# Performance work log

Hardware: AMD Instinct MI355X
Metric: run time of the kernel (lower is better)

## Reference

```python
import jax, jax.numpy as jnp
import numpy as np

FEATURE_DIM = 512
NUM_HEADS = 8
HEAD_DIM = FEATURE_DIM // NUM_HEADS


def setup_inputs() -> dict:
    key = jax.random.key(0)
    ks = jax.random.split(key, 16)
    B, N, F = 16, 768, FEATURE_DIM
    Nb = N // 3
    s = 1.0 / np.sqrt(F)
    inp = {
        "x_1": jax.random.normal(ks[0], (B, N, F), jnp.float32),
        "x_2": jax.random.normal(ks[1], (B, N, F), jnp.float32),
        "z_b": jax.random.normal(ks[2], (Nb, F), jnp.float32),
        # weights stored [in, out] (torch Linear applies x @ W.T)
        "Wqkv_i": jax.random.normal(ks[3], (F, 3 * F), jnp.float32) * s,
        "Wqkv_j": jax.random.normal(ks[4], (F, 3 * F), jnp.float32) * s,
        "Wqkv_b": jax.random.normal(ks[5], (F, 3 * F), jnp.float32) * s,
        "W_f": jax.random.normal(ks[6], (2 * F, F), jnp.float32) * s,
        "b_f": jnp.zeros((F,), jnp.float32),
        "W_m": jax.random.normal(ks[7], (F, F), jnp.float32) * s,
        "b_m": jnp.zeros((F,), jnp.float32),
        "W_QKV": jax.random.normal(ks[8], (F, 3 * F), jnp.float32) * s,
        "W_proj": jax.random.normal(ks[9], (F, F), jnp.float32) * s,
        "b_proj": jnp.zeros((F,), jnp.float32),
    }
    return inp


def reference(x_1, x_2, z_b, Wqkv_i, Wqkv_j, Wqkv_b, W_f, b_f, W_m, b_m, W_QKV, W_proj, b_proj):
    z_i, z_j = x_1, x_2
    B, N, F = z_i.shape
    Nb = z_b.shape[0]
    scale = F ** -0.5           # full-dim attention scale
    Scale = HEAD_DIM ** -0.5    # multi-head attention scale

    zb = jnp.broadcast_to((z_b * 0.2)[None], (B, Nb, F))

    def split_qkv(x, W):
        qkv = (x @ W).reshape(x.shape[0], x.shape[1], 3, F)
        return qkv[:, :, 0], qkv[:, :, 1], qkv[:, :, 2]

    _, k_i, v_i = split_qkv(z_i, Wqkv_i)
    q_j, _, _ = split_qkv(z_j, Wqkv_j)
    q_b, k_b, v_b = split_qkv(zb, Wqkv_b)

    # bottleneck cross attentions (single-head, full feature dim)
    a_ib = jax.nn.softmax(jnp.einsum('bmf,bnf->bmn', q_b, k_i) * scale, axis=-1)  # [B,Nb,N]
    a_bj = jax.nn.softmax(jnp.einsum('bnf,bmf->bnm', q_j, k_b) * scale, axis=-1)  # [B,N,Nb]

    a_ib = jnp.einsum('bmn,bnf->bmf', a_ib, v_i)  # [B,Nb,F]
    attn_up = jax.nn.softmax(jnp.einsum('bnf,bmf->bnm', z_i, a_ib) * scale, axis=-1)  # [B,N,Nb]
    a_ib = jnp.einsum('bnm,bmf->bnf', attn_up, a_ib)  # [B,N,F]
    a_bj = jnp.einsum('bnm,bmf->bnf', a_bj, v_b)      # [B,N,F]
    a_ij = (a_ib + a_bj) * 0.5

    # gated fusion
    f_ij = jax.nn.sigmoid(jnp.concatenate([a_ij, z_j], axis=-1) @ W_f + b_f)
    h_ij = jax.nn.relu(z_i + (a_ij @ W_m + b_m) * f_ij)

    # standard multi-head self-attention
    QKV = (h_ij @ W_QKV).reshape(B, N, 3, NUM_HEADS, HEAD_DIM)
    Q, K, V = [jnp.transpose(QKV[:, :, t], (0, 2, 1, 3)) for t in range(3)]  # [B,H,N,hd]
    Attn = jax.nn.softmax(jnp.einsum('bhnd,bhmd->bhnm', Q, K) * Scale, axis=-1)
    H = jnp.einsum('bhnm,bhmd->bhnd', Attn, V)
    H = jnp.transpose(H, (0, 2, 1, 3)).reshape(B, N, F)
    return H @ W_proj + b_proj
```

## Files before the change

kernel.cpp:

```cpp
#include <hip/hip_runtime.h>
#include <hip/hip_bf16.h>

typedef __attribute__((ext_vector_type(8))) short short8;
typedef __attribute__((ext_vector_type(4))) float f32x4;
typedef __hip_bfloat16 bf16;
typedef unsigned short ushort;

__device__ __forceinline__ ushort f2b(float v) {
    bf16 h = __float2bfloat16(v);
    return *reinterpret_cast<ushort*>(&h);
}
__device__ __forceinline__ float b2f(ushort u) {
    return __uint_as_float((unsigned)u << 16);
}

#define GLD16(lds, gp) __builtin_amdgcn_global_load_lds( \
    (const __attribute__((address_space(1))) void*)(gp), \
    (__attribute__((address_space(3))) void*)(lds), 16, 0, 0)

__device__ __forceinline__ void xcd_swizzle(int& bx, int& by) {
    if ((gridDim.y & 7) == 0) {
        const int id = bx + gridDim.x * by;
        const int xcd = id & 7, slot = id >> 3;
        by = xcd * (gridDim.y >> 3) + slot / gridDim.x;
        bx = slot - (slot / gridDim.x) * gridDim.x;
    }
}

template<typename OutT, int EPI, int TM>
__global__ __launch_bounds__(256) void gemm_bf16(
    const bf16* __restrict__ A, const bf16* __restrict__ B, OutT* __restrict__ C,
    int K, int lda, int ldb, int ldc, long sA, long sB, long sC,
    float alpha, const float* __restrict__ bias,
    int lda2, long sA2, int eld, long sE,
    bf16* __restrict__ px, bf16* __restrict__ py, int nry)
{
    constexpr int RT = TM / 32;
    constexpr int PLA = TM * 32;
    constexpr int PLB = 128 * 32;
    constexpr int NP = (TM == 64) ? 4 : 2;
    __shared__ __align__(16) bf16 As[NP * PLA];
    __shared__ __align__(16) bf16 Bs[NP * PLB];

    const int t = threadIdx.x;
    const int w = t >> 6, lane = t & 63;
    const int wr = w >> 1, wc = w & 1;
    const int lr = lane & 15, kc4 = lane >> 4;
    const int qr = lane >> 2;
    const int kcr = ((lane & 3) - ((lane >> 3) & 3)) & 3;
    int bx = blockIdx.x, by = blockIdx.y;
    xcd_swizzle(bx, by);
    int zidx, row0;
    if (nry > 0) { zidx = by / nry; row0 = (by % nry) * TM; }
    else         { zidx = blockIdx.z; row0 = by * TM; }
    const int col0 = bx * 128;

    const bf16* Asel = A; const bf16* Bsel = B;
    long sBe = sB, sAe = sA; int ldbe = ldb, ldae = lda;
    if constexpr (EPI == 7) {
        if (blockIdx.z == 1) {
            Asel = (const bf16*)px; Bsel = (const bf16*)py;
            sBe = 0; ldbe = eld; ldae = lda2; sAe = sA2;
        }
    }
    const bf16* Ab = Asel + (size_t)zidx * sAe + (size_t)row0 * ldae;
    const bf16* Bb = Bsel + (size_t)zidx * sBe + (size_t)col0 * ldbe;

    const bf16* ga0; const bf16* ga1 = nullptr;
    if constexpr (TM == 64) {
        ga0 = Ab + (size_t)(w * 16 + qr) * ldae + kcr * 8;
    } else {
        ga0 = Ab + (size_t)(w * 32 + qr) * ldae + kcr * 8;
        ga1 = Ab + (size_t)(w * 32 + 16 + qr) * ldae + kcr * 8;
    }
    const bf16* gb0 = Bb + (size_t)(w * 32 + qr) * ldbe + kcr * 8;
    const bf16* gb1 = Bb + (size_t)(w * 32 + 16 + qr) * ldbe + kcr * 8;
    bf16* lA0; bf16* lA1 = nullptr;
    if constexpr (TM == 64) { lA0 = &As[w * 512]; }
    else                    { lA0 = &As[w * 1024]; lA1 = &As[w * 1024 + 512]; }
    bf16* lB0 = &Bs[w * 1024];
    bf16* lB1 = &Bs[w * 1024 + 512];

    f32x4 acc[RT][4] = {};

    const int cSw = ((kc4 + ((lr >> 1) & 3)) & 3) * 8;
    const bf16* ApBase = &As[(wr * (TM / 2) + lr) * 32 + cSw];
    const bf16* BpBase = &Bs[(wc * 64 + lr) * 32 + cSw];

    auto stageP = [&](int plane, int ko) {
        GLD16(lA0 + plane * PLA, ga0 + ko);
        if constexpr (TM == 128) GLD16(lA1 + plane * PLA, ga1 + ko);
        GLD16(lB0 + plane * PLB, gb0 + ko);
        GLD16(lB1 + plane * PLB, gb1 + ko);
    };
    auto compP = [&](int plane) {
        const bf16* Ap = ApBase + plane * PLA;
        const bf16* Bp = BpBase + plane * PLB;
        short8 af[RT], bfr[4];
#pragma unroll
        for (int i = 0; i < RT; ++i) af[i]  = *(const short8*)(Ap + i * 512);
#pragma unroll
        for (int j = 0; j < 4; ++j) bfr[j] = *(const short8*)(Bp + j * 512);
#pragma unroll
        for (int i = 0; i < RT; ++i)
#pragma unroll
            for (int j = 0; j < 4; ++j)
                acc[i][j] = __builtin_amdgcn_mfma_f32_16x16x32_bf16(af[i], bfr[j], acc[i][j], 0, 0, 0);
    };

    if constexpr (TM == 64) {
        stageP(0, 0); stageP(1, 32);
        int buf = 0;
        for (int k0 = 0; k0 < K; k0 += 64) {
            __syncthreads();
            if (k0 + 64 < K) {
                stageP((buf ^ 1) * 2,     k0 + 64);
                stageP((buf ^ 1) * 2 + 1, k0 + 96);
            }
            compP(buf * 2); compP(buf * 2 + 1);
            buf ^= 1;
        }
    } else {
        stageP(0, 0);
        int buf = 0;
        for (int k0 = 0; k0 < K; k0 += 32) {
            __syncthreads();
            if (k0 + 32 < K) stageP(buf ^ 1, k0 + 32);
            compP(buf);
            buf ^= 1;
        }
    }

    if constexpr (EPI == 4) {
        const int sec = bx >> 2;
        const int h0 = (bx & 3) * 2;
        const int b  = by / 6;
        const int n0 = (by % 6) * TM;
        bf16* dq = (bf16*)C;
#pragma unroll
        for (int j = 0; j < 4; ++j) {
            const int col = wc * 64 + j * 16 + lr;
            const int h = h0 + (col >> 6), hd = col & 63;
            const size_t bh = (size_t)b * 8 + h;
#pragma unroll
            for (int i = 0; i < RT; ++i) {
                const int n = n0 + wr * (TM / 2) + i * 16 + kc4 * 4;
                if (sec == 2) {
                    __align__(8) ushort o[4];
#pragma unroll
                    for (int r = 0; r < 4; ++r) o[r] = f2b(acc[i][j][r]);
                    *(int2*)&py[(bh * 64 + hd) * 768 + n] = *(const int2*)o;
                } else {
                    bf16* d = (sec == 0) ? dq : px;
#pragma unroll
                    for (int r = 0; r < 4; ++r)
                        d[(bh * 768 + n + r) * 64 + hd] = __float2bfloat16(acc[i][j][r]);
                }
            }
        }
        return;
    } else if constexpr (EPI == 5) {
        const int b  = by / 6;
        const int n0 = (by % 6) * TM;
#pragma unroll
        for (int j = 0; j < 4; ++j) {
            const int col = col0 + wc * 64 + j * 16 + lr;
#pragma unroll
            for (int i = 0; i < RT; ++i) {
                const int n = n0 + wr * (TM / 2) + i * 16 + kc4 * 4;
                if (col < 512) {
#pragma unroll
                    for (int r = 0; r < 4; ++r)
                        ((bf16*)C)[((size_t)b * 768 + n + r) * 512 + col] = __float2bfloat16(acc[i][j][r]);
                } else {
                    __align__(8) ushort o[4];
#pragma unroll
                    for (int r = 0; r < 4; ++r) o[r] = f2b(acc[i][j][r]);
                    *(int2*)&py[((size_t)b * 512 + (col - 512)) * 768 + n] = *(const int2*)o;
                }
            }
        }
        return;
    }

    const int czid = (EPI == 7) ? (int)blockIdx.z * 16 + zidx : zidx;
    OutT* Cb = C + (size_t)czid * sC;
#pragma unroll
    for (int j = 0; j < 4; ++j) {
        const int col = col0 + wc * 64 + j * 16 + lr;
        const float bv = bias ? bias[col] : 0.f;
#pragma unroll
        for (int i = 0; i < RT; ++i) {
            const int rb = row0 + wr * (TM / 2) + i * 16 + kc4 * 4;
            if constexpr (EPI == 6) {
                __align__(8) ushort o[4];
#pragma unroll
                for (int r = 0; r < 4; ++r) {
                    o[r] = f2b(alpha * acc[i][j][r]);
                    Cb[(size_t)(rb + r) * ldc + col] = __float2bfloat16(alpha * acc[i][j][r]);
                }
                *(int2*)&py[(size_t)czid * sE + (size_t)col * eld + rb] = *(const int2*)o;
            } else if constexpr (EPI == 8) {
                __align__(8) ushort o[4];
#pragma unroll
                for (int r = 0; r < 4; ++r) {
                    o[r] = f2b(acc[i][j][r]);
                    Cb[(size_t)(rb + r) * ldc + col] = __float2bfloat16(acc[i][j][r]);
                }
                if (col >= 1024) {
                    const size_t tb = (size_t)(col - 1024) * 512 + 256 + rb;
#pragma unroll
                    for (int b2 = 0; b2 < 16; ++b2)
                        *(int2*)&py[(size_t)b2 * sE + tb] = *(const int2*)o;
                }
            } else {
#pragma unroll
                for (int r = 0; r < 4; ++r) {
                    const int row = rb + r;
                    float v = alpha * acc[i][j][r] + bv;
                    if constexpr (sizeof(OutT) == 2)
                        Cb[(size_t)row * ldc + col] = __float2bfloat16(v);
                    else
                        Cb[(size_t)row * ldc + col] = v;
                }
            }
        }
    }
}

__global__ __launch_bounds__(256) void gemm_gate(
    const bf16* __restrict__ A, const bf16* __restrict__ Bf,
    const bf16* __restrict__ Bm, bf16* __restrict__ Cout,
    const float* __restrict__ bias_f, const float* __restrict__ bias_m,
    const float* __restrict__ x1)
{
    constexpr int AHW = 64 * 32;
    constexpr int BHW = 128 * 32;
    __shared__ __align__(16) bf16 As[2 * AHW];
    __shared__ __align__(16) bf16 FsS[2 * BHW];
    __shared__ __align__(16) bf16 MsS[2 * BHW];

    const int t = threadIdx.x;
    const int w = t >> 6, lane = t & 63;
    const int lr = lane & 15, kc4 = lane >> 4;
    const int qr = lane >> 2;
    const int kcr = ((lane & 3) - ((lane >> 3) & 3)) & 3;
    int bx = blockIdx.x, by = blockIdx.y;
    xcd_swizzle(bx, by);
    const int row0 = by * 64, col0 = bx * 128;

    const bf16* ga0 = A  + (size_t)(row0 + w * 16 + qr) * 1024 + kcr * 8;
    const bf16* gf0 = Bf + (size_t)(col0 + w * 32 + qr) * 1024 + kcr * 8;
    const bf16* gf1 = Bf + (size_t)(col0 + w * 32 + 16 + qr) * 1024 + kcr * 8;
    const bf16* gm0 = Bm + (size_t)(col0 + w * 32 + qr) * 512 + kcr * 8;
    const bf16* gm1 = Bm + (size_t)(col0 + w * 32 + 16 + qr) * 512 + kcr * 8;
    bf16* lA0 = &As[w * 512];
    bf16* lF0 = &FsS[w * 1024]; bf16* lF1 = &FsS[w * 1024 + 512];
    bf16* lM0 = &MsS[w * 1024]; bf16* lM1 = &MsS[w * 1024 + 512];

    f32x4 acc1[4][2] = {};
    f32x4 acc2[4][2] = {};

    const int cSw = ((kc4 + ((lr >> 1) & 3)) & 3) * 8;
    const bf16* ApBase = &As[lr * 32 + cSw];
    const bf16* FpBase = &FsS[(w * 32 + lr) * 32 + cSw];
    const bf16* MpBase = &MsS[(w * 32 + lr) * 32 + cSw];

    GLD16(lA0, ga0);
    GLD16(lF0, gf0); GLD16(lF1, gf1);
    GLD16(lM0, gm0); GLD16(lM1, gm1);

    auto step = [&](int kk, int rd, int st) {
        __syncthreads();
        const int kn = kk + 32;
        if (kn < 1024) {
            GLD16(lA0 + st * AHW, ga0 + kn);
            GLD16(lF0 + st * BHW, gf0 + kn);
            GLD16(lF1 + st * BHW, gf1 + kn);
            if (kn < 512) {
                GLD16(lM0 + st * BHW, gm0 + kn);
                GLD16(lM1 + st * BHW, gm1 + kn);
            }
        }
        const bf16* Ap = ApBase + rd * AHW;
        const bf16* Fp = FpBase + rd * BHW;
        short8 af[4], ff[2];
#pragma unroll
        for (int i = 0; i < 4; ++i) af[i] = *(const short8*)(Ap + i * 512);
#pragma unroll
        for (int j = 0; j < 2; ++j) ff[j] = *(const short8*)(Fp + j * 512);
#pragma unroll
        for (int i = 0; i < 4; ++i)
#pragma unroll
            for (int j = 0; j < 2; ++j)
                acc1[i][j] = __builtin_amdgcn_mfma_f32_16x16x32_bf16(af[i], ff[j], acc1[i][j], 0, 0, 0);
        if (kk < 512) {
            const bf16* Mp = MpBase + rd * BHW;
            short8 mf[2];
#pragma unroll
            for (int j = 0; j < 2; ++j) mf[j] = *(const short8*)(Mp + j * 512);
#pragma unroll
            for (int i = 0; i < 4; ++i)
#pragma unroll
                for (int j = 0; j < 2; ++j)
                    acc2[i][j] = __builtin_amdgcn_mfma_f32_16x16x32_bf16(af[i], mf[j], acc2[i][j], 0, 0, 0);
        }
    };

    for (int k0 = 0; k0 < 1024; k0 += 64) {
        step(k0, 0, 1);
        step(k0 + 32, 1, 0);
    }

#pragma unroll
    for (int j = 0; j < 2; ++j) {
        const int col = col0 + w * 32 + j * 16 + lr;
        const float bvf = bias_f[col], bvm = bias_m[col];
#pragma unroll
        for (int i = 0; i < 4; ++i) {
            const int rb = row0 + i * 16 + kc4 * 4;
#pragma unroll
            for (int r = 0; r < 4; ++r) {
                const int row = rb + r;
                const float sig = 1.f / (1.f + __expf(-(acc1[i][j][r] + bvf)));
                const float rr = x1[(size_t)row * 512 + col] + (acc2[i][j][r] + bvm) * sig;
                Cout[(size_t)row * 512 + col] = __float2bfloat16(rr > 0.f ? rr : 0.f);
            }
        }
    }
}

template<typename TI, int NSRC>
__global__ __launch_bounds__(256) void k_transpose(
    const TI* __restrict__ s0, const TI* __restrict__ s1,
    const TI* __restrict__ s2, const TI* __restrict__ s3,
    bf16* __restrict__ dst, int src_ld, int dst_ld, long sSrc, long sDst,
    int rep, long repStride)
{
    __shared__ float tile[64][65];
    const int t = threadIdx.x;
    const int c0 = blockIdx.x * 64, r0 = blockIdx.y * 64;
    const int z = blockIdx.z;
    const TI* src = s0;
    if (NSRC > 1) src = (z == 0) ? s0 : (z == 1) ? s1 : (z == 2) ? s2 : s3;
    {
        const int r = t >> 2, cq = (t & 3) * 16;
        const TI* sp = src + (size_t)z * sSrc + (size_t)(r0 + r) * src_ld + c0 + cq;
        if constexpr (sizeof(TI) == 4) {
#pragma unroll
            for (int u = 0; u < 16; u += 4) {
                float4 v = *(const float4*)((const float*)sp + u);
                tile[r][cq + u]     = v.x; tile[r][cq + u + 1] = v.y;
                tile[r][cq + u + 2] = v.z; tile[r][cq + u + 3] = v.w;
            }
        } else {
            const ushort* up = (const ushort*)sp;
            union { short8 v; ushort u[8]; } p0, p1;
            p0.v = *(const short8*)up; p1.v = *(const short8*)(up + 8);
#pragma unroll
            for (int u = 0; u < 8; ++u) {
                tile[r][cq + u]     = b2f(p0.u[u]);
                tile[r][cq + 8 + u] = b2f(p1.u[u]);
            }
        }
    }
    __syncthreads();
    const int c = t >> 2, rq = (t & 3) * 16;
    __align__(16) ushort ob[16];
#pragma unroll
    for (int u = 0; u < 16; ++u) ob[u] = f2b(tile[rq + u][c]);
    for (int rp = 0; rp < rep; ++rp) {
        bf16* dp = dst + (size_t)rp * repStride + (size_t)z * sDst + (size_t)(c0 + c) * dst_ld + r0 + rq;
        *(int4*)dp       = *(const int4*)&ob[0];
        *(int4*)(dp + 8) = *(const int4*)&ob[8];
    }
}

__global__ __launch_bounds__(256) void k_cast3(const float* __restrict__ x1,
    const float* __restrict__ x2, const float* __restrict__ zb,
    const float* __restrict__ wj,
    bf16* __restrict__ d1, bf16* __restrict__ d2, bf16* __restrict__ d3,
    bf16* __restrict__ d4)
{
    const int z = blockIdx.z;
    const float* src; bf16* dst; int ld; float scale; int n;
    if (z == 0)      { src = x1; dst = d1; ld = 512;  scale = 1.f;  n = 6291456; }
    else if (z == 1) { src = x2; dst = d2; ld = 1024; scale = 1.f;  n = 6291456; }
    else if (z == 2) { src = zb; dst = d3; ld = 512;  scale = 0.2f; n = 131072;  }
    else             { src = wj; dst = d4; ld = 512;  scale = 1.f;  n = 262144;  }
    int i = (blockIdx.x * 256 + threadIdx.x) * 8;
    if (i >= n) return;
    int si = i;
    if (z == 3) si = (i >> 9) * 1536 + (i & 511);
    float4 a = *(const float4*)(src + si), b = *(const float4*)(src + si + 4);
    __align__(16) ushort o[8];
    o[0] = f2b(a.x * scale); o[1] = f2b(a.y * scale); o[2] = f2b(a.z * scale); o[3] = f2b(a.w * scale);
    o[4] = f2b(b.x * scale); o[5] = f2b(b.y * scale); o[6] = f2b(b.z * scale); o[7] = f2b(b.w * scale);
    int row = i >> 9, col = i & 511;
    *(int4*)(dst + (size_t)row * ld + col) = *(const int4*)o;
}

template<int COLS, int MODE>
__global__ __launch_bounds__(256) void softmax_wave(const float* __restrict__ X,
                                                    bf16* __restrict__ Y)
{
    const int wv = threadIdx.x >> 6, lane = threadIdx.x & 63;
    const long row = (long)blockIdx.x * 4 + wv;
    const float* src = X + row * COLS;
    constexpr int V = COLS / 64;
    float v[V];
#pragma unroll
    for (int i = 0; i < V; ++i) v[i] = src[lane + i * 64];
    float m = v[0];
#pragma unroll
    for (int i = 1; i < V; ++i) m = fmaxf(m, v[i]);
#pragma unroll
    for (int o = 32; o; o >>= 1) m = fmaxf(m, __shfl_xor(m, o));
    float s = 0.f;
#pragma unroll
    for (int i = 0; i < V; ++i) { v[i] = __expf(v[i] - m); s += v[i]; }
#pragma unroll
    for (int o = 32; o; o >>= 1) s += __shfl_xor(s, o);
    const float inv = 1.f / s;
    bf16* dst;
    if constexpr (MODE == 0) {
        dst = Y + row * COLS;
    } else {
        const int z = (int)(row / 768), mm = (int)(row % 768);
        dst = Y + ((size_t)(z & 15) * 768 + mm) * 512 + (z >> 4) * 256;
    }
#pragma unroll
    for (int i = 0; i < V; ++i) dst[lane + i * 64] = __float2bfloat16(v[i] * inv);
}

__global__ __launch_bounds__(256) void mhsa_flash_mfma(
    const bf16* __restrict__ Qb, const bf16* __restrict__ Kb,
    const bf16* __restrict__ VT, bf16* __restrict__ Hout)
{
    constexpr int LD = 72;
    __shared__ __align__(16) ushort Qs[64 * LD];
    __shared__ __align__(16) ushort Ks[64 * LD];
    __shared__ __align__(16) ushort Vt[64 * LD];
    __shared__ __align__(16) ushort Ps[64 * LD];

    const int t = threadIdx.x;
    const int w = t >> 6, lane = t & 63;
    const int l16 = lane & 15, q4 = lane >> 4;
    const int h = blockIdx.x, b = blockIdx.y, qt = blockIdx.z;
    const size_t bh = (size_t)b * 8 + h;
    const ushort* qbase = (const ushort*)Qb + bh * 768 * 64;
    const ushort* kbase = (const ushort*)Kb + bh * 768 * 64;
    const ushort* vbase = (const ushort*)VT + bh * 64 * 768;

    const int r = t >> 2, c0 = (t & 3) * 16;

    {
        const ushort* src = qbase + (size_t)(qt * 64 + r) * 64 + c0;
        *(int4*)&Qs[r * LD + c0]     = *(const int4*)src;
        *(int4*)&Qs[r * LD + c0 + 8] = *(const int4*)(src + 8);
    }

    int4 ka0, ka1, va0, va1;
    {
        const ushort* ks = kbase + (size_t)r * 64 + c0;
        ka0 = *(const int4*)ks; ka1 = *(const int4*)(ks + 8);
        const ushort* vs = vbase + (size_t)r * 768 + c0;
        va0 = *(const int4*)vs; va1 = *(const int4*)(vs + 8);
    }
    __syncthreads();

    short8 qf0 = *(const short8*)&Qs[(w * 16 + l16) * LD + q4 * 8];
    short8 qf1 = *(const short8*)&Qs[(w * 16 + l16) * LD + 32 + q4 * 8];

    float lsum[4] = {0.f, 0.f, 0.f, 0.f};
    f32x4 acc[4] = {};

    for (int kt = 0; kt < 12; ++kt) {
        if (kt) __syncthreads();
        *(int4*)&Ks[r * LD + c0]     = ka0;
        *(int4*)&Ks[r * LD + c0 + 8] = ka1;
        *(int4*)&Vt[r * LD + c0]     = va0;
        *(int4*)&Vt[r * LD + c0 + 8] = va1;
        __syncthreads();

        if (kt < 11) {
            const ushort* ks = kbase + (size_t)((kt + 1) * 64 + r) * 64 + c0;
            ka0 = *(const int4*)ks; ka1 = *(const int4*)(ks + 8);
            const ushort* vs = vbase + (size_t)r * 768 + (kt + 1) * 64 + c0;
            va0 = *(const int4*)vs; va1 = *(const int4*)(vs + 8);
        }

        f32x4 s[4] = {};
#pragma unroll
        for (int nt = 0; nt < 4; ++nt) {
            short8 kf0 = *(const short8*)&Ks[(nt * 16 + l16) * LD + q4 * 8];
            short8 kf1 = *(const short8*)&Ks[(nt * 16 + l16) * LD + 32 + q4 * 8];
            s[nt] = __builtin_amdgcn_mfma_f32_16x16x32_bf16(qf0, kf0, s[nt], 0, 0, 0);
            s[nt] = __builtin_amdgcn_mfma_f32_16x16x32_bf16(qf1, kf1, s[nt], 0, 0, 0);
        }

#pragma unroll
        for (int nt = 0; nt < 4; ++nt) {
#pragma unroll
            for (int e = 0; e < 4; ++e) {
                const float p = __expf(s[nt][e] * 0.125f);
                lsum[e] += p;
                Ps[(w * 16 + q4 * 4 + e) * LD + nt * 16 + l16] = f2b(p);
            }
        }

        short8 pf0 = *(const short8*)&Ps[(w * 16 + l16) * LD + q4 * 8];
        short8 pf1 = *(const short8*)&Ps[(w * 16 + l16) * LD + 32 + q4 * 8];
#pragma unroll
        for (int jt = 0; jt < 4; ++jt) {
            short8 vf0 = *(const short8*)&Vt[(jt * 16 + l16) * LD + q4 * 8];
            short8 vf1 = *(const short8*)&Vt[(jt * 16 + l16) * LD + 32 + q4 * 8];
            acc[jt] = __builtin_amdgcn_mfma_f32_16x16x32_bf16(pf0, vf0, acc[jt], 0, 0, 0);
            acc[jt] = __builtin_amdgcn_mfma_f32_16x16x32_bf16(pf1, vf1, acc[jt], 0, 0, 0);
        }
    }

    const int orow = qt * 64 + w * 16 + q4 * 4;
#pragma unroll
    for (int e = 0; e < 4; ++e) {
        float l = lsum[e];
        l += __shfl_xor(l, 1);
        l += __shfl_xor(l, 2);
        l += __shfl_xor(l, 4);
        l += __shfl_xor(l, 8);
        const float inv = 1.f / l;
        const size_t rbase = ((size_t)b * 768 + orow + e) * 512 + h * 64;
#pragma unroll
        for (int jt = 0; jt < 4; ++jt)
            Hout[rbase + jt * 16 + l16] = __float2bfloat16(acc[jt][e] * inv);
    }
}

extern "C" void kernel_launch(void* const* d_in, const int* in_sizes, int n_in,
                              void* d_out, int out_size, void* d_ws, size_t ws_size,
                              hipStream_t stream)
{
    (void)in_sizes; (void)n_in; (void)out_size; (void)ws_size;
    const float* x1     = (const float*)d_in[0];
    const float* x2     = (const float*)d_in[1];
    const float* z_b    = (const float*)d_in[2];
    const float* Wqkv_i = (const float*)d_in[3];
    const float* Wqkv_j = (const float*)d_in[4];
    const float* Wqkv_b = (const float*)d_in[5];
    const float* W_f    = (const float*)d_in[6];
    const float* b_f    = (const float*)d_in[7];
    const float* W_m    = (const float*)d_in[8];
    const float* b_m    = (const float*)d_in[9];
    const float* W_QKV  = (const float*)d_in[10];
    const float* W_proj = (const float*)d_in[11];
    const float* b_proj = (const float*)d_in[12];
    float* out = (float*)d_out;

    const float scale = 0.044194173824159216f;

    char* base = (char*)d_ws;
    size_t off = 0;
    auto alloc = [&](size_t bytes) { char* r = base + off; off += (bytes + 255) & ~(size_t)255; return r; };

    char* Rq  = alloc((size_t)3 * 25165824);
    char* R1  = Rq;
    char* R2  = Rq + 25165824;
    char* R3  = Rq + 2 * 25165824;
    char* R4  = alloc(25165824);
    bf16* Wt4     = (bf16*)alloc((size_t)3 * 1536 * 512 * 2);
    bf16* Wt_f    = (bf16*)alloc(512 * 1024 * 2);
    bf16* Wt_mp   = (bf16*)alloc((size_t)2 * 512 * 512 * 2);
    bf16* Wj_bf   = (bf16*)alloc(512 * 512 * 2);
    bf16* Gbuf    = (bf16*)alloc(256 * 512 * 2);
    bf16* c_zb    = (bf16*)alloc(256 * 512 * 2);
    bf16* qkvb    = (bf16*)alloc(256 * 1536 * 2);
    bf16* aib0    = (bf16*)alloc((size_t)16 * 256 * 512 * 2);
    bf16* Bcat    = (bf16*)alloc((size_t)16 * 512 * 512 * 2);
    float* S      = (float*)alloc((size_t)32 * 768 * 256 * 4);
    bf16* Sb1     = (bf16*)alloc((size_t)16 * 256 * 768 * 2);
    bf16* Sb_cat  = (bf16*)alloc((size_t)16 * 768 * 512 * 2);
    bf16* c_cat   = (bf16*)alloc((size_t)12288 * 1024 * 2);
    bf16* hbuf    = (bf16*)alloc((size_t)12288 * 512 * 2);

    bf16* Wt_i = Wt4, *Wt_b = Wt4 + 1536 * 512,
        *Wt_qkv = Wt4 + (size_t)2 * 1536 * 512;
    bf16* Wt_m = Wt_mp, *Wt_proj = Wt_mp + 512 * 512;

    bf16*  Kc   = (bf16*)R1;
    bf16*  Qb   = (bf16*)R1;
    bf16*  Kb   = (bf16*)(R1 + 12582912);
    bf16*  v_iT = (bf16*)R2;
    bf16*  VTb  = (bf16*)R2;
    bf16*  c_x1 = (bf16*)R3;
    bf16*  Hout = (bf16*)R4;

    auto G64 = [&](const bf16* A, const bf16* B, void* C, bool outBf,
                   int M, int N, int K, int lda, int ldb, int ldc,
                   long sA, long sB, long sC, int batch, float alpha,
                   const float* bias) {
        int nry = M / 64;
        dim3 grid(N / 128, (batch > 1) ? batch * nry : nry, 1);
        if (batch == 1) nry = 0;
        if (outBf) gemm_bf16<bf16, 0, 64><<<grid, 256, 0, stream>>>(A, B, (bf16*)C, K, lda, ldb, ldc, sA, sB, sC, alpha, bias, 0, 0, 0, 0, nullptr, nullptr, nry);
        else       gemm_bf16<float, 0, 64><<<grid, 256, 0, stream>>>(A, B, (float*)C, K, lda, ldb, ldc, sA, sB, sC, alpha, bias, 0, 0, 0, 0, nullptr, nullptr, nry);
    };

    k_cast3<<<dim3(3072, 1, 4), 256, 0, stream>>>(x1, x2, z_b, Wqkv_j,
                                                  c_x1, c_cat + 512, c_zb, Wj_bf);
    k_transpose<float, 3><<<dim3(24, 8, 3), 256, 0, stream>>>(
        Wqkv_i, Wqkv_b, W_QKV, nullptr, Wt4, 1536, 512, 0, 1536L * 512, 1, 0);
    k_transpose<float, 1><<<dim3(8, 16, 1), 256, 0, stream>>>(
        W_f, nullptr, nullptr, nullptr, Wt_f, 512, 1024, 0, 0, 1, 0);
    k_transpose<float, 2><<<dim3(8, 8, 2), 256, 0, stream>>>(
        W_m, W_proj, nullptr, nullptr, Wt_mp, 512, 512, 0, 512L * 512, 1, 0);

    gemm_bf16<bf16, 8, 64><<<dim3(12, 4, 1), 256, 0, stream>>>(
        c_zb, Wt_b, qkvb, 512, 512, 512, 1536, 0, 0, 0,
        1.f, nullptr, 0, 0, 0, 512L * 512, nullptr, Bcat, 0);
    G64(qkvb + 512, Wj_bf, Gbuf, true, 256, 512, 512, 1536, 512, 512, 0, 0, 0, 1, 1.f, nullptr);
    gemm_bf16<bf16, 5, 128><<<dim3(8, 96, 1), 256, 0, stream>>>(
        c_x1, Wt_i + 512 * 512, Kc, 512, 512, 512, 512, 0, 0, 0,
        1.f, nullptr, 0, 0, 0, 0, nullptr, v_iT, 0);
    G64(qkvb, Kc, S, false, 256, 768, 512, 1536, 512, 768, 0, 768L * 512, 256L * 768, 16, scale, nullptr);
    softmax_wave<768, 0><<<1024, 256, 0, stream>>>(S, Sb1);
    gemm_bf16<bf16, 6, 64><<<dim3(4, 64, 1), 256, 0, stream>>>(
        Sb1, v_iT, aib0, 768, 768, 768, 512, 256L * 768, 512L * 768, 256L * 512,
        1.f, nullptr, 0, 0, 512, 512L * 512, nullptr, Bcat, 4);
    gemm_bf16<float, 7, 64><<<dim3(2, 192, 2), 256, 0, stream>>>(
        c_x1, aib0, S, 512, 512, 512, 256, 768L * 512, 256L * 512, 768L * 256,
        scale, nullptr, 1024, 768L * 1024, 512, 0,
        c_cat + 512, Gbuf, 12);
    softmax_wave<256, 1><<<6144, 256, 0, stream>>>(S, Sb_cat);
    G64(Sb_cat, Bcat, c_cat, true, 768, 512, 512, 512, 512, 1024,
        768L * 512, 512L * 512, 768L * 1024, 16, 0.5f, nullptr);
    gemm_gate<<<dim3(4, 192), 256, 0, stream>>>(c_cat, Wt_f, Wt_m, hbuf, b_f, b_m, x1);
    gemm_bf16<bf16, 4, 128><<<dim3(12, 96, 1), 256, 0, stream>>>(
        hbuf, Wt_qkv, Qb, 512, 512, 512, 0, 0, 0, 0,
        1.f, nullptr, 0, 0, 0, 0, Kb, VTb, 0);
    mhsa_flash_mfma<<<dim3(8, 16, 12), 256, 0, stream>>>(Qb, Kb, VTb, Hout);
    G64(Hout, Wt_proj, out, false, 12288, 512, 512, 512, 512, 512, 0, 0, 0, 1, 1.f, b_proj);
}
```

Measured before the change: 382.4 us.

## Fuse attn_up/bottleneck score GEMM with row softmax into one kernel

Replaces the EPI-7 GEMM that wrote fp32 scores to a scratch buffer, and the separate 256-wide softmax pass, with a new gemm_sm kernel. Each block computes a full 64x256 score tile across two waves per row and combines max and sum through shared memory. It then writes normalized bf16 probabilities straight into Sb_cat, removing the fp32 round trip and one launch. The gate kernel also reads x1 from the existing bf16 copy instead of fp32, which cuts bandwidth but slightly lowers precision of the residual.

```diff
diff --git a/kernel.cpp b/kernel.cpp
--- a/kernel.cpp
+++ b/kernel.cpp
@@ -55,26 +55,18 @@
     else         { zidx = blockIdx.z; row0 = by * TM; }
     const int col0 = bx * 128;
 
-    const bf16* Asel = A; const bf16* Bsel = B;
-    long sBe = sB, sAe = sA; int ldbe = ldb, ldae = lda;
-    if constexpr (EPI == 7) {
-        if (blockIdx.z == 1) {
-            Asel = (const bf16*)px; Bsel = (const bf16*)py;
-            sBe = 0; ldbe = eld; ldae = lda2; sAe = sA2;
-        }
-    }
-    const bf16* Ab = Asel + (size_t)zidx * sAe + (size_t)row0 * ldae;
-    const bf16* Bb = Bsel + (size_t)zidx * sBe + (size_t)col0 * ldbe;
+    const bf16* Ab = A + (size_t)zidx * sA + (size_t)row0 * lda;
+    const bf16* Bb = B + (size_t)zidx * sB + (size_t)col0 * ldb;
 
     const bf16* ga0; const bf16* ga1 = nullptr;
     if constexpr (TM == 64) {
-        ga0 = Ab + (size_t)(w * 16 + qr) * ldae + kcr * 8;
+        ga0 = Ab + (size_t)(w * 16 + qr) * lda + kcr * 8;
     } else {
-        ga0 = Ab + (size_t)(w * 32 + qr) * ldae + kcr * 8;
-        ga1 = Ab + (size_t)(w * 32 + 16 + qr) * ldae + kcr * 8;
-    }
-    const bf16* gb0 = Bb + (size_t)(w * 32 + qr) * ldbe + kcr * 8;
-    const bf16* gb1 = Bb + (size_t)(w * 32 + 16 + qr) * ldbe + kcr * 8;
+        ga0 = Ab + (size_t)(w * 32 + qr) * lda + kcr * 8;
+        ga1 = Ab + (size_t)(w * 32 + 16 + qr) * lda + kcr * 8;
+    }
+    const bf16* gb0 = Bb + (size_t)(w * 32 + qr) * ldb + kcr * 8;
+    const bf16* gb1 = Bb + (size_t)(w * 32 + 16 + qr) * ldb + kcr * 8;
     bf16* lA0; bf16* lA1 = nullptr;
     if constexpr (TM == 64) { lA0 = &As[w * 512]; }
     else                    { lA0 = &As[w * 1024]; lA1 = &As[w * 1024 + 512]; }
@@ -183,8 +175,7 @@
         return;
     }
 
-    const int czid = (EPI == 7) ? (int)blockIdx.z * 16 + zidx : zidx;
-    OutT* Cb = C + (size_t)czid * sC;
+    OutT* Cb = C + (size_t)zidx * sC;
 #pragma unroll
     for (int j = 0; j < 4; ++j) {
         const int col = col0 + wc * 64 + j * 16 + lr;
@@ -199,7 +190,7 @@
                     o[r] = f2b(alpha * acc[i][j][r]);
                     Cb[(size_t)(rb + r) * ldc + col] = __float2bfloat16(alpha * acc[i][j][r]);
                 }
-                *(int2*)&py[(size_t)czid * sE + (size_t)col * eld + rb] = *(const int2*)o;
+                *(int2*)&py[(size_t)zidx * sE + (size_t)col * eld + rb] = *(const int2*)o;
             } else if constexpr (EPI == 8) {
                 __align__(8) ushort o[4];
 #pragma unroll
@@ -228,11 +219,134 @@
     }
 }
 
+__global__ __launch_bounds__(256) void gemm_sm(
+    const bf16* __restrict__ A0, const bf16* __restrict__ B0,
+    const bf16* __restrict__ A1, const bf16* __restrict__ B1,
+    bf16* __restrict__ Y, float alpha)
+{
+    constexpr int PLA = 64 * 32;
+    constexpr int PLB = 256 * 32;
+    __shared__ __align__(16) bf16 As[2 * PLA];
+    __shared__ __align__(16) bf16 Bs[2 * PLB];
+    __shared__ float sc[2][2][2][32];
+
+    const int t = threadIdx.x;
+    const int w = t >> 6, lane = t & 63;
+    const int wr = w >> 1, wc = w & 1;
+    const int lr = lane & 15, kc4 = lane >> 4;
+    const int qr = lane >> 2;
+    const int kcr = ((lane & 3) - ((lane >> 3) & 3)) & 3;
+    int bx = blockIdx.x, by = blockIdx.y;
+    xcd_swizzle(bx, by);
+    const int b = by / 12, row0 = (by % 12) * 64;
+    const int half = blockIdx.z;
+
+    const bf16* Ab; int lda; const bf16* Bb;
+    if (half == 0) {
+        Ab = A0 + (size_t)b * (768L * 512) + (size_t)row0 * 512;  lda = 512;
+        Bb = B0 + (size_t)b * (256L * 512);
+    } else {
+        Ab = A1 + (size_t)b * (768L * 1024) + (size_t)row0 * 1024; lda = 1024;
+        Bb = B1;
+    }
+
+    const bf16* ga0 = Ab + (size_t)(w * 16 + qr) * lda + kcr * 8;
+    const bf16* gb0 = Bb + (size_t)(w * 32 + qr) * 512 + kcr * 8;
+    const bf16* gb1 = Bb + (size_t)(w * 32 + 16 + qr) * 512 + kcr * 8;
+    const bf16* gb2 = Bb + (size_t)(128 + w * 32 + qr) * 512 + kcr * 8;
+    const bf16* gb3 = Bb + (size_t)(128 + w * 32 + 16 + qr) * 512 + kcr * 8;
+    bf16* lA0 = &As[w * 512];
+    bf16* lB0 = &Bs[w * 1024];        bf16* lB1 = &Bs[w * 1024 + 512];
+    bf16* lB2 = &Bs[4096 + w * 1024]; bf16* lB3 = &Bs[4096 + w * 1024 + 512];
+
+    f32x4 acc[2][8] = {};
+
+    const int cSw = ((kc4 + ((lr >> 1) & 3)) & 3) * 8;
+    const bf16* ApBase = &As[(wr * 32 + lr) * 32 + cSw];
+    const bf16* BpBase = &Bs[(wc * 128 + lr) * 32 + cSw];
+
+    auto stageP = [&](int pl, int ko) {
+        GLD16(lA0 + pl * PLA, ga0 + ko);
+        GLD16(lB0 + pl * PLB, gb0 + ko); GLD16(lB1 + pl * PLB, gb1 + ko);
+        GLD16(lB2 + pl * PLB, gb2 + ko); GLD16(lB3 + pl * PLB, gb3 + ko);
+    };
+    auto compP = [&](int pl) {
+        const bf16* Ap = ApBase + pl * PLA;
+        const bf16* Bp = BpBase + pl * PLB;
+        short8 af[2], bfr[8];
+#pragma unroll
+        for (int i = 0; i < 2; ++i) af[i] = *(const short8*)(Ap + i * 512);
+#pragma unroll
+        for (int j = 0; j < 8; ++j) bfr[j] = *(const short8*)(Bp + j * 512);
+#pragma unroll
+        for (int i = 0; i < 2; ++i)
+#pragma unroll
+            for (int j = 0; j < 8; ++j)
+                acc[i][j] = __builtin_amdgcn_mfma_f32_16x16x32_bf16(af[i], bfr[j], acc[i][j], 0, 0, 0);
+    };
+
+    stageP(0, 0);
+    int buf = 0;
+    for (int k0 = 0; k0 < 512; k0 += 32) {
+        __syncthreads();
+        if (k0 + 32 < 512) stageP(buf ^ 1, k0 + 32);
+        compP(buf);
+        buf ^= 1;
+    }
+
+    float mloc[2][4], sloc[2][4], scl[2][4];
+#pragma unroll
+    for (int i = 0; i < 2; ++i)
+#pragma unroll
+        for (int e = 0; e < 4; ++e) {
+            float m = alpha * acc[i][0][e];
+#pragma unroll
+            for (int j = 1; j < 8; ++j) m = fmaxf(m, alpha * acc[i][j][e]);
+#pragma unroll
+            for (int o = 1; o < 16; o <<= 1) m = fmaxf(m, __shfl_xor(m, o));
+            mloc[i][e] = m;
+            float s = 0.f;
+#pragma unroll
+            for (int j = 0; j < 8; ++j) {
+                const float p = __expf(alpha * acc[i][j][e] - m);
+                acc[i][j][e] = p;
+                s += p;
+            }
+#pragma unroll
+            for (int o = 1; o < 16; o <<= 1) s += __shfl_xor(s, o);
+            sloc[i][e] = s;
+            if (lr == 0) {
+                sc[wr][wc][0][i * 16 + kc4 * 4 + e] = m;
+                sc[wr][wc][1][i * 16 + kc4 * 4 + e] = s;
+            }
+        }
+    __syncthreads();
+#pragma unroll
+    for (int i = 0; i < 2; ++i)
+#pragma unroll
+        for (int e = 0; e < 4; ++e) {
+            const float m2 = sc[wr][wc ^ 1][0][i * 16 + kc4 * 4 + e];
+            const float s2 = sc[wr][wc ^ 1][1][i * 16 + kc4 * 4 + e];
+            const float M = fmaxf(mloc[i][e], m2);
+            const float S = sloc[i][e] * __expf(mloc[i][e] - M) + s2 * __expf(m2 - M);
+            scl[i][e] = __expf(mloc[i][e] - M) / S;
+        }
+    bf16* dst = Y + ((size_t)b * 768 + row0) * 512 + half * 256 + wc * 128;
+#pragma unroll
+    for (int i = 0; i < 2; ++i)
+#pragma unroll
+        for (int j = 0; j < 8; ++j)
+#pragma unroll
+            for (int e = 0; e < 4; ++e)
+                dst[(size_t)(wr * 32 + i * 16 + kc4 * 4 + e) * 512 + j * 16 + lr] =
+                    __float2bfloat16(acc[i][j][e] * scl[i][e]);
+}
+
 __global__ __launch_bounds__(256) void gemm_gate(
     const bf16* __restrict__ A, const bf16* __restrict__ Bf,
     const bf16* __restrict__ Bm, bf16* __restrict__ Cout,
     const float* __restrict__ bias_f, const float* __restrict__ bias_m,
-    const float* __restrict__ x1)
+    const bf16* __restrict__ x1b)
 {
     constexpr int AHW = 64 * 32;
     constexpr int BHW = 128 * 32;
@@ -312,6 +426,7 @@
         step(k0 + 32, 1, 0);
     }
 
+    const ushort* xr = (const ushort*)x1b;
 #pragma unroll
     for (int j = 0; j < 2; ++j) {
         const int col = col0 + w * 32 + j * 16 + lr;
@@ -323,7 +438,7 @@
             for (int r = 0; r < 4; ++r) {
                 const int row = rb + r;
                 const float sig = 1.f / (1.f + __expf(-(acc1[i][j][r] + bvf)));
-                const float rr = x1[(size_t)row * 512 + col] + (acc2[i][j][r] + bvm) * sig;
+                const float rr = b2f(xr[(size_t)row * 512 + col]) + (acc2[i][j][r] + bvm) * sig;
                 Cout[(size_t)row * 512 + col] = __float2bfloat16(rr > 0.f ? rr : 0.f);
             }
         }
@@ -422,13 +537,7 @@
 #pragma unroll
     for (int o = 32; o; o >>= 1) s += __shfl_xor(s, o);
     const float inv = 1.f / s;
-    bf16* dst;
-    if constexpr (MODE == 0) {
-        dst = Y + row * COLS;
-    } else {
-        const int z = (int)(row / 768), mm = (int)(row % 768);
-        dst = Y + ((size_t)(z & 15) * 768 + mm) * 512 + (z >> 4) * 256;
-    }
+    bf16* dst = Y + row * COLS;
 #pragma unroll
     for (int i = 0; i < V; ++i) dst[lane + i * 64] = __float2bfloat16(v[i] * inv);
 }
@@ -576,7 +685,7 @@
     bf16* qkvb    = (bf16*)alloc(256 * 1536 * 2);
     bf16* aib0    = (bf16*)alloc((size_t)16 * 256 * 512 * 2);
     bf16* Bcat    = (bf16*)alloc((size_t)16 * 512 * 512 * 2);
-    float* S      = (float*)alloc((size_t)32 * 768 * 256 * 4);
+    float* S      = (float*)alloc((size_t)16 * 256 * 768 * 4);
     bf16* Sb1     = (bf16*)alloc((size_t)16 * 256 * 768 * 2);
     bf16* Sb_cat  = (bf16*)alloc((size_t)16 * 768 * 512 * 2);
     bf16* c_cat   = (bf16*)alloc((size_t)12288 * 1024 * 2);
@@ -626,14 +735,11 @@
     gemm_bf16<bf16, 6, 64><<<dim3(4, 64, 1), 256, 0, stream>>>(
         Sb1, v_iT, aib0, 768, 768, 768, 512, 256L * 768, 512L * 768, 256L * 512,
         1.f, nullptr, 0, 0, 512, 512L * 512, nullptr, Bcat, 4);
-    gemm_bf16<float, 7, 64><<<dim3(2, 192, 2), 256, 0, stream>>>(
-        c_x1, aib0, S, 512, 512, 512, 256, 768L * 512, 256L * 512, 768L * 256,
-        scale, nullptr, 1024, 768L * 1024, 512, 0,
-        c_cat + 512, Gbuf, 12);
-    softmax_wave<256, 1><<<6144, 256, 0, stream>>>(S, Sb_cat);
+    gemm_sm<<<dim3(1, 192, 2), 256, 0, stream>>>(c_x1, aib0, c_cat + 512, Gbuf,
+                                                 Sb_cat, scale);
     G64(Sb_cat, Bcat, c_cat, true, 768, 512, 512, 512, 512, 1024,
         768L * 512, 512L * 512, 768L * 1024, 16, 0.5f, nullptr);
-    gemm_gate<<<dim3(4, 192), 256, 0, stream>>>(c_cat, Wt_f, Wt_m, hbuf, b_f, b_m, x1);
+    gemm_gate<<<dim3(4, 192), 256, 0, stream>>>(c_cat, Wt_f, Wt_m, hbuf, b_f, b_m, c_x1);
     gemm_bf16<bf16, 4, 128><<<dim3(12, 96, 1), 256, 0, stream>>>(
         hbuf, Wt_qkv, Qb, 512, 512, 512, 0, 0, 0, 0,
         1.f, nullptr, 0, 0, 0, 0, Kb, VTb, 0);
```

After: 383.4 us. About the same (+0.3%).
